# Kernel tuning notes

Hardware: AMD Instinct MI355X
Metric: run time of the kernel (lower is better)

The kernel has to match this reference:

```python
import jax, jax.numpy as jnp
import numpy as np

EPS = 1e-5

def _inorm(t):
    # InstanceNorm2d, affine=False: normalize each (B,C) plane over H,W
    m = t.mean((2, 3), keepdims=True)
    v = t.var((2, 3), keepdims=True)
    return (t - m) * jax.lax.rsqrt(v + EPS)

def _conv(x, w, b):
    y = jax.lax.conv_general_dilated(x, w, (1, 1), 'SAME',
        dimension_numbers=('NCHW', 'OIHW', 'NCHW'))
    return y + b[None, :, None, None]

def _ss2d(xh, in_proj_w, conv_w, conv_b, x_proj_w, dt_w, dt_b, A_logs, Ds,
          out_norm_g, out_norm_b, out_proj_w):
    # xh: (B,H,W,C) -> (B,H,W,C). VMamba-style 4-direction selective scan.
    B, H, W, C = xh.shape
    Di = in_proj_w.shape[0] // 2
    n = A_logs.shape[-1]
    R = dt_w.shape[-1]
    L = H * W
    xz = xh @ in_proj_w.T                      # (B,H,W,2*Di)
    xin, z = xz[..., :Di], xz[..., Di:]
    xc = xin.transpose(0, 3, 1, 2)             # (B,Di,H,W)
    xc = jax.lax.conv_general_dilated(xc, conv_w, (1, 1), 'SAME',
        feature_group_count=Di, dimension_numbers=('NCHW', 'OIHW', 'NCHW'))
    xc = jax.nn.silu(xc + conv_b[None, :, None, None])
    x1 = xc.reshape(B, Di, L)                  # row-major scan
    x2 = xc.transpose(0, 1, 3, 2).reshape(B, Di, L)  # col-major scan
    xs = jnp.stack([x1, x2, x1[..., ::-1], x2[..., ::-1]], axis=1)  # (B,4,Di,L)
    x_dbl = jnp.einsum('bkdl,kcd->bkcl', xs, x_proj_w)
    dts = jnp.einsum('bkrl,kdr->bkdl', x_dbl[:, :, :R], dt_w)
    Bs, Cs = x_dbl[:, :, R:R + n], x_dbl[:, :, R + n:]
    delta = jax.nn.softplus(dts + dt_b[None, :, :, None])
    A = -jnp.exp(A_logs)                       # (4,Di,n)
    scan_in = (jnp.moveaxis(xs, -1, 0), jnp.moveaxis(delta, -1, 0),
               jnp.moveaxis(Bs, -1, 0), jnp.moveaxis(Cs, -1, 0))
    def step(h, inp):
        u, d, b, c = inp                       # u,d:(B,4,Di)  b,c:(B,4,n)
        h = jnp.exp(d[..., None] * A) * h + (d * u)[..., None] * b[:, :, None, :]
        return h, (h * c[:, :, None, :]).sum(-1)
    h0 = jnp.zeros((B, 4, Di, n), xh.dtype)
    _, ys = jax.lax.scan(step, h0, scan_in)    # ys: (L,B,4,Di)
    out_y = jnp.moveaxis(ys, 0, -1) + Ds[None, :, :, None] * xs  # (B,4,Di,L)
    def _wh(t):
        return t.reshape(B, Di, W, H).transpose(0, 1, 3, 2).reshape(B, Di, L)
    y = out_y[:, 0] + out_y[:, 2, :, ::-1] + _wh(out_y[:, 1]) + _wh(out_y[:, 3, :, ::-1])
    y = y.transpose(0, 2, 1).reshape(B, H, W, Di)
    mu = y.mean(-1, keepdims=True)
    v = y.var(-1, keepdims=True)
    y = (y - mu) * jax.lax.rsqrt(v + EPS) * out_norm_g + out_norm_b
    return (y * jax.nn.silu(z)) @ out_proj_w.T

def setup_inputs():
    key = jax.random.key(0)
    ks = jax.random.split(key, 16)
    B, C, H, W = 4, 96, 64, 64
    Di, n, R, K, SQ, CC = 192, 8, 6, 4, 16, 16
    f = jnp.float32
    nrm = lambda k, s: 0.02 * jax.random.normal(k, s, dtype=f)
    inp = {}
    inp['x'] = jax.random.normal(ks[0], (B, C, H, W), dtype=f)
    inp['dz'] = jax.random.uniform(ks[1], (B, 1, H, W), dtype=f)
    inp['in_proj_w'] = nrm(ks[2], (2 * Di, C))
    inp['conv_w'] = nrm(ks[3], (Di, 1, 3, 3))
    inp['conv_b'] = jnp.zeros((Di,), f)
    inp['x_proj_w'] = nrm(ks[4], (K, R + 2 * n, Di))
    inp['dt_w'] = nrm(ks[5], (K, Di, R))
    inp['dt_b'] = 0.01 * jnp.ones((K, Di), f)
    inp['A_logs'] = jnp.log(jnp.tile(jnp.arange(1, n + 1, dtype=f)[None, None, :], (K, Di, 1)))
    inp['Ds'] = jnp.ones((K, Di), f)
    inp['out_norm_g'] = jnp.ones((Di,), f)
    inp['out_norm_b'] = jnp.zeros((Di,), f)
    inp['out_proj_w'] = nrm(ks[6], (C, Di))
    inp['ln_g'] = jnp.ones((C,), f)
    inp['ln_b'] = jnp.zeros((C,), f)
    inp['skip_ss2d'] = jnp.ones((C,), f)
    inp['cca_w1'] = nrm(ks[7], (SQ, C))
    inp['cca_b1'] = jnp.zeros((SQ,), f)
    inp['cca_w2'] = nrm(ks[8], (C, SQ))
    inp['cca_b2'] = jnp.zeros((C,), f)
    inp['bnc_w1'] = nrm(ks[9], (CC, C, 1, 1))
    inp['bnc_b1'] = jnp.zeros((CC,), f)
    inp['bnc_w2'] = nrm(ks[10], (CC, CC, 3, 3))
    inp['bnc_b2'] = jnp.zeros((CC,), f)
    inp['bnc_w3'] = nrm(ks[11], (C, CC, 1, 1))
    inp['bnc_b3'] = jnp.zeros((C,), f)
    return inp

def reference(x, dz, in_proj_w, conv_w, conv_b, x_proj_w, dt_w, dt_b, A_logs, Ds,
              out_norm_g, out_norm_b, out_proj_w, ln_g, ln_b, skip_ss2d,
              cca_w1, cca_b1, cca_w2, cca_b2,
              bnc_w1, bnc_b1, bnc_w2, bnc_b2, bnc_w3, bnc_b3):
    SKIP_CCA, SKIP_BNC = 0.4, 1.0
    # 1) channel cross-attention block (dz-guided SE), residual w/ skip 0.4
    xn = _inorm(x)
    pooled = (xn * dz).sum((2, 3)) / (dz.sum((2, 3)) + 1e-6)  # (B,C)
    s = jax.nn.sigmoid(jax.nn.relu(pooled @ cca_w1.T + cca_b1) @ cca_w2.T + cca_b2)
    x = xn * s[:, :, None, None] + SKIP_CCA * x
    # 2) SS2D block in NHWC, residual w/ learned per-channel skip weight
    xh = x.transpose(0, 2, 3, 1)
    mu = xh.mean(-1, keepdims=True)
    v = xh.var(-1, keepdims=True)
    xln = (xh - mu) * jax.lax.rsqrt(v + EPS) * ln_g + ln_b
    y = _ss2d(xln, in_proj_w, conv_w, conv_b, x_proj_w, dt_w, dt_b, A_logs, Ds,
              out_norm_g, out_norm_b, out_proj_w)
    x = (y + skip_ss2d * xh).transpose(0, 3, 1, 2)
    # 3) bottleneck conv block, residual w/ skip 1.0
    xn = _inorm(x)
    h = jax.nn.relu(_conv(xn, bnc_w1, bnc_b1))
    h = jax.nn.relu(_conv(h, bnc_w2, bnc_b2))
    h = _conv(h, bnc_w3, bnc_b3)
    return h + SKIP_BNC * x
```

## Files before the change

kernel.cpp:

```cpp
#include <hip/hip_runtime.h>
#include <hip/hip_bf16.h>
#include <math.h>

constexpr int TOT_IN = 1685008;

constexpr size_t F_x    = 64;
constexpr size_t F_dz   = F_x + 1572864;
constexpr size_t F_ipw  = F_dz + 16384;
constexpr size_t F_convw= F_ipw + 36864;
constexpr size_t F_convb= F_convw + 1728;
constexpr size_t F_xpw  = F_convb + 192;
constexpr size_t F_dtw  = F_xpw + 16896;
constexpr size_t F_dtb  = F_dtw + 4608;
constexpr size_t F_alog = F_dtb + 768;
constexpr size_t F_Dsv  = F_alog + 6144;
constexpr size_t F_ong  = F_Dsv + 768;
constexpr size_t F_onb  = F_ong + 192;
constexpr size_t F_opw  = F_onb + 192;
constexpr size_t F_lng  = F_opw + 18432;
constexpr size_t F_lnb  = F_lng + 96;
constexpr size_t F_skip = F_lnb + 96;
constexpr size_t F_cw1  = F_skip + 96;
constexpr size_t F_cb1  = F_cw1 + 1536;
constexpr size_t F_cw2  = F_cb1 + 16;
constexpr size_t F_cb2  = F_cw2 + 1536;
constexpr size_t F_bw1  = F_cb2 + 96;
constexpr size_t F_bb1  = F_bw1 + 1536;
constexpr size_t F_bw2  = F_bb1 + 16;
constexpr size_t F_bb2  = F_bw2 + 2304;
constexpr size_t F_bw3  = F_bb2 + 16;
constexpr size_t F_bb3  = F_bw3 + 1536;
constexpr size_t F_stat = 1685504;
constexpr size_t F_mean1= F_stat;
constexpr size_t F_rstd1= F_stat + 384;
constexpr size_t F_wsum = F_stat + 768;
constexpr size_t F_sca  = F_stat + 1216;
constexpr size_t F_mean2= F_stat + 1664;
constexpr size_t F_rstd2= F_stat + 2048;
constexpr size_t F_xcca = 1689600;
constexpr size_t F_xln  = F_xcca + 1572864;
constexpr size_t F_xin  = F_xln  + 1572864;
constexpr size_t F_z    = F_xin  + 3145728;
constexpr size_t F_xct  = F_z    + 3145728;
constexpr size_t F_xdbl = F_xct  + 3145728;
constexpr size_t F_old1 = F_xdbl + 1572864;
constexpr size_t F_xccaT= F_old1 + 3145728;
constexpr size_t F_yc   = F_xccaT+ 1572864;
constexpr size_t F_tb   = F_yc   + 3145728;
constexpr size_t F_x2   = F_tb   + 3145728;
constexpr size_t F_h1   = F_x2   + 1572864;
constexpr size_t F_h2   = F_h1   + 262144;
constexpr size_t F_xpwt = F_h2   + 262144;
constexpr size_t F_ipwt = F_xpwt + 18432;
constexpr size_t F_opwt = F_ipwt + 36864;
constexpr size_t F_cwt  = F_opwt + 18432;
constexpr size_t F_hend = F_xin;
constexpr size_t F_apr  = F_tb;
constexpr size_t F_hcar = F_old1;

__constant__ int g_off[27] = {
  0,1572864,1589248,1626112,1627840,1628032,1644928,1649536,1650304,1656448,
  1657216,1657408,1657600,1676032,1676128,1676224,1676320,1677856,1677872,1679408,
  1679504,1681040,1681056,1683360,1683376,1684912,1685008};

struct Ptrs26 { const void* p[26]; };

static __device__ __forceinline__ float sigmoidf_(float x){ return 1.f/(1.f+__expf(-x)); }
static __device__ __forceinline__ float siluf_(float x){ return x*sigmoidf_(x); }
static __device__ __forceinline__ float softplusf_(float x){ return x>15.f ? x : log1pf(__expf(x)); }
static __device__ __forceinline__ int mapk_(int k,int l){
  switch(k){
    case 0: return l;
    case 1: return ((l&63)<<6)|(l>>6);
    case 2: return 4095-l;
    default:{ int l2=4095-l; return ((l2&63)<<6)|(l2>>6); }
  }
}

__global__ void k_convert(Ptrs26 ps, float* __restrict__ F){
  int bf = (((const unsigned int*)ps.p[9])[0] == 0x3F803F80u) ? 1 : 0;
  int stride = gridDim.x*blockDim.x;
  for (int idx = blockIdx.x*blockDim.x+threadIdx.x; idx < TOT_IN; idx += stride){
    int lo = 0, hi = 26;
    while (hi - lo > 1){ int mid = (lo+hi)>>1; if (idx >= g_off[mid]) lo = mid; else hi = mid; }
    int s = lo;
    int loc = idx - g_off[s];
    float v;
    if (bf) v = __bfloat162float(((const __hip_bfloat16*)ps.p[s])[loc]);
    else    v = ((const float*)ps.p[s])[loc];
    F[64 + idx] = v;
  }
}

__global__ void k_wtrans(float* __restrict__ F){
  int idx = blockIdx.x*256 + threadIdx.x;
  if (idx < 18432){
    int c = idx % 24; int d = (idx/24) % 192; int k = idx/(24*192);
    F[F_xpwt + idx] = (c < 22) ? F[F_xpw + (size_t)(k*22 + c)*192 + d] : 0.f;
  } else if (idx < 18432 + 36864){
    int i = idx - 18432;
    int j = i % 384, c = i / 384;
    F[F_ipwt + i] = F[F_ipw + (size_t)j*96 + c];
  } else if (idx < 18432 + 36864 + 18432){
    int i = idx - 18432 - 36864;
    int c = i % 96, d = i / 96;
    F[F_opwt + i] = F[F_opw + (size_t)c*192 + d];
  } else if (idx < 18432 + 36864 + 18432 + 1728){
    int i = idx - 18432 - 36864 - 18432;
    int d = i % 192, tap = i / 192;
    F[F_cwt + i] = F[F_convw + (size_t)d*9 + tap];
  }
}

__global__ void k_inorm1(float* __restrict__ F){
  int bc = blockIdx.x; int b = bc/96;
  const float* xp  = F + F_x  + (size_t)bc*4096;
  const float* dzp = F + F_dz + (size_t)b*4096;
  float s=0.f, s2=0.f, sw=0.f;
  for (int l=threadIdx.x; l<4096; l+=256){ float v=xp[l]; s+=v; s2+=v*v; sw+=v*dzp[l]; }
  for (int m=32;m;m>>=1){ s+=__shfl_xor(s,m); s2+=__shfl_xor(s2,m); sw+=__shfl_xor(sw,m); }
  __shared__ float red[12];
  int wid = threadIdx.x>>6;
  if ((threadIdx.x&63)==0){ red[wid]=s; red[4+wid]=s2; red[8+wid]=sw; }
  __syncthreads();
  if (threadIdx.x==0){
    s = red[0]+red[1]+red[2]+red[3];
    s2= red[4]+red[5]+red[6]+red[7];
    sw= red[8]+red[9]+red[10]+red[11];
    float mean = s*(1.f/4096.f);
    float var  = s2*(1.f/4096.f) - mean*mean;
    F[F_mean1+bc]=mean; F[F_rstd1+bc]=rsqrtf(var+1e-5f); F[F_wsum+bc]=sw;
  }
}

__global__ void k_cca(float* __restrict__ F){
  __shared__ float ps[96], hid[16], red[2];
  int b = blockIdx.x, t = threadIdx.x;
  const float* dzp = F + F_dz + (size_t)b*4096;
  float s=0.f;
  for (int l=t; l<4096; l+=128) s += dzp[l];
  for (int m=32;m;m>>=1) s += __shfl_xor(s,m);
  if ((t&63)==0) red[t>>6] = s;
  __syncthreads();
  float dzs = red[0]+red[1];
  if (t<96){
    int bc = b*96+t;
    ps[t] = F[F_rstd1+bc]*(F[F_wsum+bc]-F[F_mean1+bc]*dzs)/(dzs+1e-6f);
  }
  __syncthreads();
  if (t<16){
    float a = F[F_cb1+t];
    for (int c=0;c<96;c++) a += ps[c]*F[F_cw1+t*96+c];
    hid[t] = fmaxf(a,0.f);
  }
  __syncthreads();
  if (t<96){
    float a = F[F_cb2+t];
    for (int j=0;j<16;j++) a += hid[j]*F[F_cw2+t*16+j];
    F[F_sca+b*96+t] = sigmoidf_(a);
  }
}

__global__ __launch_bounds__(256) void k_ccat(float* __restrict__ F){
  __shared__ float T[96*33];
  int b = blockIdx.x >> 7; int l0 = (blockIdx.x & 127)*32;
  for (int i = threadIdx.x; i < 3072; i += 256){
    int l = i & 31, c = i >> 5;
    int bc = b*96 + c;
    float v = F[F_x + (size_t)bc*4096 + l0 + l];
    float xv = (v - F[F_mean1+bc])*F[F_rstd1+bc]*F[F_sca+bc] + 0.4f*v;
    F[F_xcca + (size_t)bc*4096 + l0 + l] = xv;
    T[c*33 + l] = xv;
  }
  __syncthreads();
  for (int i = threadIdx.x; i < 3072; i += 256){
    int c = i % 96, l = i / 96;
    F[F_xccaT + ((size_t)(b*4096 + l0 + l))*96 + c] = T[c*33 + l];
  }
}

__global__ __launch_bounds__(128) void k_gemm1(
    const float* __restrict__ xt, const float* __restrict__ lng,
    const float* __restrict__ lnb, const float* __restrict__ wt1,
    float* __restrict__ xin, float* __restrict__ z)
{
  int lb = blockIdx.x & 127; int jc = blockIdx.x >> 7;
  int t = lb*128 + threadIdx.x;
  const float4* rp = (const float4*)(xt + (size_t)t*96);
  float s=0.f, s2=0.f;
  for (int c4=0; c4<24; c4++){
    float4 v = rp[c4];
    s  += v.x+v.y+v.z+v.w;
    s2 += v.x*v.x+v.y*v.y+v.z*v.z+v.w*v.w;
  }
  float mean = s*(1.f/96.f);
  float rstd = rsqrtf(s2*(1.f/96.f) - mean*mean + 1e-5f);
  const float4* gp = (const float4*)lng;
  const float4* bp = (const float4*)lnb;
  const float* wbase = wt1 + jc*24;
  float acc[24];
  #pragma unroll
  for (int j=0;j<24;j++) acc[j]=0.f;
  for (int c4=0; c4<24; c4++){
    float4 av = rp[c4]; float4 g = gp[c4]; float4 bb = bp[c4];
    float tv[4];
    tv[0] = (av.x-mean)*rstd*g.x + bb.x;
    tv[1] = (av.y-mean)*rstd*g.y + bb.y;
    tv[2] = (av.z-mean)*rstd*g.z + bb.z;
    tv[3] = (av.w-mean)*rstd*g.w + bb.w;
    #pragma unroll
    for (int cc=0; cc<4; cc++){
      const float* wr = wbase + (size_t)(c4*4+cc)*384;
      #pragma unroll
      for (int j=0;j<24;j++) acc[j] += tv[cc] * wr[j];
    }
  }
  float* op = (jc < 8) ? (xin + (size_t)t*192 + jc*24)
                       : (z   + (size_t)t*192 + (jc-8)*24);
  float4* o4 = (float4*)op;
  #pragma unroll
  for (int q=0;q<6;q++) o4[q] = make_float4(acc[q*4],acc[q*4+1],acc[q*4+2],acc[q*4+3]);
}

__global__ void k_dwconv(const float* __restrict__ xin, const float* __restrict__ cwt,
                         const float* __restrict__ cb, float* __restrict__ xct){
  int idx = blockIdx.x*256 + threadIdx.x;
  if (idx >= 786432) return;
  int d4 = idx % 48; int bl = idx / 48; int l = bl & 4095; int b = bl >> 12;
  int h = l >> 6, w = l & 63;
  const float4* xp = (const float4*)(xin + (size_t)b*4096*192);
  const float4* wp = (const float4*)cwt;
  float4 bias = ((const float4*)cb)[d4];
  float ax=bias.x, ay=bias.y, az=bias.z, aw=bias.w;
  #pragma unroll
  for (int ky=0; ky<3; ky++){
    int hh = h + ky - 1; if ((unsigned)hh > 63u) continue;
    #pragma unroll
    for (int kx=0; kx<3; kx++){
      int ww = w + kx - 1; if ((unsigned)ww > 63u) continue;
      float4 xv = xp[(size_t)(hh*64+ww)*48 + d4];
      float4 wv = wp[(ky*3+kx)*48 + d4];
      ax += xv.x*wv.x; ay += xv.y*wv.y; az += xv.z*wv.z; aw += xv.w*wv.w;
    }
  }
  float4 o;
  o.x = ax*sigmoidf_(ax); o.y = ay*sigmoidf_(ay);
  o.z = az*sigmoidf_(az); o.w = aw*sigmoidf_(aw);
  ((float4*)xct)[idx] = o;
}

__global__ __launch_bounds__(256) void k_xdbl(
    const float* __restrict__ xct, const float* __restrict__ wt,
    float* __restrict__ xdbl)
{
  int lb = blockIdx.x & 15; int bk = blockIdx.x >> 4;
  int b = bk >> 2, k = bk & 3;
  int l = lb*256 + threadIdx.x;
  int sp = mapk_(k, l);
  const float4* rp = (const float4*)(xct + ((size_t)b*4096 + sp)*192);
  const float* wk = wt + (size_t)k*192*24;
  float acc[24];
  #pragma unroll
  for (int c=0;c<24;c++) acc[c]=0.f;
  #pragma unroll 2
  for (int d4=0; d4<48; d4++){
    float4 av = rp[d4];
    #pragma unroll
    for (int j=0;j<4;j++){
      float ad = (j==0)?av.x:(j==1)?av.y:(j==2)?av.z:av.w;
      const float* wd = wk + (d4*4+j)*24;
      #pragma unroll
      for (int c=0;c<22;c++) acc[c] += ad * wd[c];
    }
  }
  acc[22]=0.f; acc[23]=0.f;
  float4* op = (float4*)(xdbl + ((size_t)bk*4096 + l)*24);
  #pragma unroll
  for (int q=0;q<6;q++) op[q] = make_float4(acc[q*4],acc[q*4+1],acc[q*4+2],acc[q*4+3]);
}

__global__ __launch_bounds__(192) void k_scan1(
    const float* __restrict__ xdbl, const float* __restrict__ xct,
    const float* __restrict__ alogs, const float* __restrict__ dtws,
    const float* __restrict__ dtbs,
    float* __restrict__ hend, float* __restrict__ apr)
{
  int chunk = blockIdx.x & 127; int bk = blockIdx.x >> 7;
  int b = bk >> 2, k = bk & 3; int d = threadIdx.x;
  const float* alog = alogs + (size_t)(k*192+d)*8;
  float A_[8], hh[8], ap[8];
  #pragma unroll
  for (int i=0;i<8;i++){ A_[i] = -__expf(alog[i]); hh[i]=0.f; ap[i]=1.f; }
  bool structured = fabsf(A_[0] + 1.f) < 1e-4f;
  #pragma unroll
  for (int i=1;i<8;i++) structured = structured && (fabsf(A_[i] - (float)(i+1)*A_[0]) <= 1e-4f*fabsf(A_[i]));
  float dtw_[6];
  #pragma unroll
  for (int r=0;r<6;r++) dtw_[r] = dtws[(size_t)(k*192+d)*6 + r];
  float dtb_ = dtbs[k*192 + d];
  const float* xB = xdbl + ((size_t)bk*4096 + chunk*32)*24;
  const float* xc = xct + (size_t)b*4096*192 + d;
  if (structured){
    #pragma unroll 4
    for (int s=0;s<32;s++){
      const float* xl = xB + s*24;
      float dt = dtb_;
      #pragma unroll
      for (int r=0;r<6;r++) dt += xl[r]*dtw_[r];
      int sp = mapk_(k, chunk*32+s);
      float u = xc[(size_t)sp*192];
      float t = __expf(dt);
      float a1 = __builtin_amdgcn_rcpf(1.f + t);
      float delta = (dt > 15.f) ? dt : __logf(1.f + t);
      float du = delta*u;
      float a = a1;
      #pragma unroll
      for (int i=0;i<8;i++){
        hh[i] = a*hh[i] + du*xl[6+i];
        ap[i] *= a;
        a *= a1;
      }
    }
  } else {
    for (int s=0;s<32;s++){
      const float* xl = xB + s*24;
      float dt = dtb_;
      #pragma unroll
      for (int r=0;r<6;r++) dt += xl[r]*dtw_[r];
      int sp = mapk_(k, chunk*32+s);
      float u = xc[(size_t)sp*192];
      float delta = softplusf_(dt);
      float du = delta*u;
      #pragma unroll
      for (int i=0;i<8;i++){
        float a = __expf(delta*A_[i]);
        hh[i] = a*hh[i] + du*xl[6+i];
        ap[i] *= a;
      }
    }
  }
  size_t base = ((size_t)(bk<<7) + chunk)*1536 + d*8;
  #pragma unroll
  for (int i=0;i<8;i++){ hend[base+i]=hh[i]; apr[base+i]=ap[i]; }
}

__global__ void k_carry(const float* __restrict__ hend, const float* __restrict__ apr,
                        float* __restrict__ hcar){
  int t = blockIdx.x*256 + threadIdx.x;
  if (t >= 16*1536) return;
  int di8 = t % 1536; int bk = t / 1536;
  float carry = 0.f;
  for (int c=0;c<128;c++){
    size_t idx = ((size_t)(bk<<7) + c)*1536 + di8;
    hcar[idx] = carry;
    carry = apr[idx]*carry + hend[idx];
  }
}

__global__ __launch_bounds__(192) void k_scan2(
    const float* __restrict__ xdbl, const float* __restrict__ xct,
    const float* __restrict__ alogs, const float* __restrict__ dtws,
    const float* __restrict__ dtbs, const float* __restrict__ Dsv,
    const float* __restrict__ hcar, float* __restrict__ ycg)
{
  int chunk = blockIdx.x & 127; int bk = blockIdx.x >> 7;
  int b = bk >> 2, k = bk & 3; int d = threadIdx.x;
  const float* alog = alogs + (size_t)(k*192+d)*8;
  float A_[8], hh[8];
  size_t cb = ((size_t)(bk<<7) + chunk)*1536 + d*8;
  #pragma unroll
  for (int i=0;i<8;i++){ A_[i] = -__expf(alog[i]); hh[i] = hcar[cb+i]; }
  bool structured = fabsf(A_[0] + 1.f) < 1e-4f;
  #pragma unroll
  for (int i=1;i<8;i++) structured = structured && (fabsf(A_[i] - (float)(i+1)*A_[0]) <= 1e-4f*fabsf(A_[i]));
  float dtw_[6];
  #pragma unroll
  for (int r=0;r<6;r++) dtw_[r] = dtws[(size_t)(k*192+d)*6 + r];
  float dtb_ = dtbs[k*192 + d];
  float Dsc  = Dsv[k*192 + d];
  const float* xB = xdbl + ((size_t)bk*4096 + chunk*32)*24;
  const float* xc = xct + (size_t)b*4096*192 + d;
  float* yc = ycg + (size_t)b*4096*192 + d;
  if (structured){
    #pragma unroll 4
    for (int s=0;s<32;s++){
      const float* xl = xB + s*24;
      float dt = dtb_;
      #pragma unroll
      for (int r=0;r<6;r++) dt += xl[r]*dtw_[r];
      int sp = mapk_(k, chunk*32+s);
      float u = xc[(size_t)sp*192];
      float t = __expf(dt);
      float a1 = __builtin_amdgcn_rcpf(1.f + t);
      float delta = (dt > 15.f) ? dt : __logf(1.f + t);
      float du = delta*u;
      float a = a1, y = 0.f;
      #pragma unroll
      for (int i=0;i<8;i++){
        hh[i] = a*hh[i] + du*xl[6+i];
        y += hh[i]*xl[14+i];
        a *= a1;
      }
      atomicAdd(&yc[(size_t)sp*192], y + Dsc*u);
    }
  } else {
    for (int s=0;s<32;s++){
      const float* xl = xB + s*24;
      float dt = dtb_;
      #pragma unroll
      for (int r=0;r<6;r++) dt += xl[r]*dtw_[r];
      int sp = mapk_(k, chunk*32+s);
      float u = xc[(size_t)sp*192];
      float delta = softplusf_(dt);
      float du = delta*u;
      float y = 0.f;
      #pragma unroll
      for (int i=0;i<8;i++){
        float a = __expf(delta*A_[i]);
        hh[i] = a*hh[i] + du*xl[6+i];
        y += hh[i]*xl[14+i];
      }
      atomicAdd(&yc[(size_t)sp*192], y + Dsc*u);
    }
  }
}

__global__ void k_tnorm(float* __restrict__ F){
  int wid = threadIdx.x >> 6, lane = threadIdx.x & 63;
  int p = blockIdx.x*4 + wid;
  size_t base = (size_t)p*192;
  const float* yc = F + F_yc;
  float v[3]; float s=0.f, s2=0.f;
  #pragma unroll
  for (int j=0;j<3;j++){ v[j]=yc[base+j*64+lane]; s+=v[j]; s2+=v[j]*v[j]; }
  for (int m=32;m;m>>=1){ s+=__shfl_xor(s,m); s2+=__shfl_xor(s2,m); }
  float mean = s*(1.f/192.f);
  float rstd = rsqrtf(s2*(1.f/192.f) - mean*mean + 1e-5f);
  #pragma unroll
  for (int j=0;j<3;j++){
    int dd = j*64+lane;
    float zv = F[F_z + base + dd];
    float t = (v[j]-mean)*rstd*F[F_ong+dd] + F[F_onb+dd];
    F[F_tb + base + dd] = t * siluf_(zv);
  }
}

__global__ __launch_bounds__(128) void k_gemm2(
    const float* __restrict__ tb, const float* __restrict__ wt2,
    const float* __restrict__ skip, const float* __restrict__ xcca,
    float* __restrict__ x2)
{
  int lb = blockIdx.x & 127; int cbk = blockIdx.x >> 7;
  int t = lb*128 + threadIdx.x;
  int b = t >> 12, l = t & 4095;
  const float4* rp = (const float4*)(tb + (size_t)t*192);
  const float* wbase = wt2 + cbk*12;
  float acc[12];
  #pragma unroll
  for (int c=0;c<12;c++) acc[c]=0.f;
  #pragma unroll 2
  for (int d4=0; d4<48; d4++){
    float4 av = rp[d4];
    #pragma unroll
    for (int dd=0; dd<4; dd++){
      float ad = (dd==0)?av.x:(dd==1)?av.y:(dd==2)?av.z:av.w;
      const float* wr = wbase + (size_t)(d4*4+dd)*96;
      #pragma unroll
      for (int c=0;c<12;c++) acc[c] += ad * wr[c];
    }
  }
  #pragma unroll
  for (int c=0;c<12;c++){
    int cg = cbk*12 + c;
    size_t o = ((size_t)(b*96+cg))*4096 + l;
    x2[o] = acc[c] + skip[cg]*xcca[o];
  }
}

__global__ void k_inorm2(float* __restrict__ F){
  int bc = blockIdx.x;
  const float* xp = F + F_x2 + (size_t)bc*4096;
  float s=0.f, s2=0.f;
  for (int l=threadIdx.x; l<4096; l+=256){ float v=xp[l]; s+=v; s2+=v*v; }
  for (int m=32;m;m>>=1){ s+=__shfl_xor(s,m); s2+=__shfl_xor(s2,m); }
  __shared__ float red[8];
  int wid = threadIdx.x>>6;
  if ((threadIdx.x&63)==0){ red[wid]=s; red[4+wid]=s2; }
  __syncthreads();
  if (threadIdx.x==0){
    s = red[0]+red[1]+red[2]+red[3];
    s2= red[4]+red[5]+red[6]+red[7];
    float mean = s*(1.f/4096.f);
    float var  = s2*(1.f/4096.f) - mean*mean;
    F[F_mean2+bc]=mean; F[F_rstd2+bc]=rsqrtf(var+1e-5f);
  }
}

__global__ void k_bnc1(float* __restrict__ F){
  int idx = blockIdx.x*256 + threadIdx.x;
  if (idx >= 4*16*4096) return;
  int l = idx & 4095; int bj = idx >> 12; int j = bj % 16; int b = bj / 16;
  float acc = F[F_bb1 + j];
  const float* wp = F + F_bw1 + j*96;
  for (int c=0;c<96;c++){
    int bc = b*96+c;
    float xn = (F[F_x2 + (size_t)bc*4096 + l] - F[F_mean2+bc])*F[F_rstd2+bc];
    acc += xn*wp[c];
  }
  F[F_h1+idx] = fmaxf(acc, 0.f);
}

__global__ void k_bnc2(float* __restrict__ F){
  int idx = blockIdx.x*256 + threadIdx.x;
  if (idx >= 4*16*4096) return;
  int l = idx & 4095; int bj = idx >> 12; int j = bj % 16; int b = bj / 16;
  int h = l >> 6, w = l & 63;
  float acc = F[F_bb2 + j];
  const float* h1p = F + F_h1 + (size_t)b*16*4096;
  const float* wp  = F + F_bw2 + j*16*9;
  for (int jp=0; jp<16; jp++){
    #pragma unroll
    for (int ky=0; ky<3; ky++){
      int hh = h + ky - 1; if (hh < 0 || hh > 63) continue;
      #pragma unroll
      for (int kx=0; kx<3; kx++){
        int ww = w + kx - 1; if (ww < 0 || ww > 63) continue;
        acc += h1p[(size_t)jp*4096 + hh*64+ww] * wp[jp*9 + ky*3 + kx];
      }
    }
  }
  F[F_h2+idx] = fmaxf(acc, 0.f);
}

__global__ void k_bnc3(float* __restrict__ F, void* __restrict__ out, const unsigned int* __restrict__ ds){
  int idx = blockIdx.x*256 + threadIdx.x;
  if (idx >= 1572864) return;
  int l = idx & 4095; int bc = idx >> 12; int c = bc % 96; int b = bc / 96;
  float acc = F[F_bb3 + c];
  const float* h2p = F + F_h2 + (size_t)b*16*4096 + l;
  const float* wp  = F + F_bw3 + c*16;
  #pragma unroll
  for (int j=0;j<16;j++) acc += h2p[(size_t)j*4096]*wp[j];
  float res = acc + F[F_x2+idx];
  if (ds[0]==0x3F803F80u) ((__hip_bfloat16*)out)[idx] = __float2bfloat16(res);
  else                    ((float*)out)[idx] = res;
}

extern "C" void kernel_launch(void* const* d_in, const int* in_sizes, int n_in,
                              void* d_out, int out_size, void* d_ws, size_t ws_size,
                              hipStream_t stream) {
  (void)in_sizes; (void)n_in; (void)out_size; (void)ws_size;
  float* F = (float*)d_ws;

  Ptrs26 ps;
  for (int i=0;i<26;i++) ps.p[i] = d_in[i];

  k_convert<<<2048, 256, 0, stream>>>(ps, F);
  hipMemsetAsync((char*)d_ws + F_yc*sizeof(float), 0, 3145728*sizeof(float), stream);
  k_wtrans<<<296, 256, 0, stream>>>(F);

  k_inorm1<<<384, 256, 0, stream>>>(F);
  k_cca   <<<4,   128, 0, stream>>>(F);
  k_ccat  <<<512, 256, 0, stream>>>(F);
  k_gemm1 <<<2048,128, 0, stream>>>(F+F_xccaT, F+F_lng, F+F_lnb, F+F_ipwt, F+F_xin, F+F_z);
  k_dwconv<<<3072,256, 0, stream>>>(F+F_xin, F+F_cwt, F+F_convb, F+F_xct);
  k_xdbl  <<<256, 256, 0, stream>>>(F+F_xct, F+F_xpwt, F+F_xdbl);
  k_scan1 <<<2048,192, 0, stream>>>(F+F_xdbl, F+F_xct, F+F_alog, F+F_dtw, F+F_dtb,
                                    F+F_hend, F+F_apr);
  k_carry <<<96,  256, 0, stream>>>(F+F_hend, F+F_apr, F+F_hcar);
  k_scan2 <<<2048,192, 0, stream>>>(F+F_xdbl, F+F_xct, F+F_alog, F+F_dtw, F+F_dtb,
                                    F+F_Dsv, F+F_hcar, F+F_yc);
  k_tnorm <<<4096,256, 0, stream>>>(F);
  k_gemm2 <<<1024,128, 0, stream>>>(F+F_tb, F+F_opwt, F+F_skip, F+F_xcca, F+F_x2);
  k_inorm2<<<384, 256, 0, stream>>>(F);
  k_bnc1  <<<1024,256, 0, stream>>>(F);
  k_bnc2  <<<1024,256, 0, stream>>>(F);
  k_bnc3  <<<6144,256, 0, stream>>>(F, d_out, (const unsigned int*)d_in[9]);
}
```

Measured before the change: 385.3 us.

## Replace scan atomics with per-direction scan-order buffers summed in tnorm

Each direction of the selective scan now writes its output plainly, in scan order, into its own buffer instead of doing atomicAdd into a shared spatial buffer. The normalization kernel gathers the four directional contributions with the inverse index mappings and sums them. This removes the zero-fill memset and the atomic contention and scattered writes. The cost is extra workspace traffic, since tnorm reads four buffers instead of one. The hard-coded offsets reuse workspace regions (including xct, which tnorm then overwrites), so correctness depends on those regions being dead at that point.

```diff
diff --git a/kernel.cpp b/kernel.cpp
--- a/kernel.cpp
+++ b/kernel.cpp
@@ -58,6 +58,12 @@
 constexpr size_t F_apr  = F_tb;
 constexpr size_t F_hcar = F_old1;
 
+__constant__ int y4off[16] = {
+  3262464, 4048896, 4835328, 5621760, 6408192, 7194624,
+  18991104, 19777536,
+  20563968, 21350400, 22136832, 22923264,
+  23709696, 24496128, 25282560, 26068992};
+
 __constant__ int g_off[27] = {
   0,1572864,1589248,1626112,1627840,1628032,1644928,1649536,1650304,1656448,
   1657216,1657408,1657600,1676032,1676128,1676224,1676320,1677856,1677872,1679408,
@@ -361,7 +367,7 @@
     const float* __restrict__ xdbl, const float* __restrict__ xct,
     const float* __restrict__ alogs, const float* __restrict__ dtws,
     const float* __restrict__ dtbs, const float* __restrict__ Dsv,
-    const float* __restrict__ hcar, float* __restrict__ ycg)
+    const float* __restrict__ hcar, float* __restrict__ yout)
 {
   int chunk = blockIdx.x & 127; int bk = blockIdx.x >> 7;
   int b = bk >> 2, k = bk & 3; int d = threadIdx.x;
@@ -380,7 +386,7 @@
   float Dsc  = Dsv[k*192 + d];
   const float* xB = xdbl + ((size_t)bk*4096 + chunk*32)*24;
   const float* xc = xct + (size_t)b*4096*192 + d;
-  float* yc = ycg + (size_t)b*4096*192 + d;
+  float* yo = yout + (size_t)y4off[bk] + ((size_t)(chunk*32))*192 + d;
   if (structured){
     #pragma unroll 4
     for (int s=0;s<32;s++){
@@ -401,7 +407,7 @@
         y += hh[i]*xl[14+i];
         a *= a1;
       }
-      atomicAdd(&yc[(size_t)sp*192], y + Dsc*u);
+      yo[(size_t)s*192] = y + Dsc*u;
     }
   } else {
     for (int s=0;s<32;s++){
@@ -420,7 +426,7 @@
         hh[i] = a*hh[i] + du*xl[6+i];
         y += hh[i]*xl[14+i];
       }
-      atomicAdd(&yc[(size_t)sp*192], y + Dsc*u);
+      yo[(size_t)s*192] = y + Dsc*u;
     }
   }
 }
@@ -428,20 +434,29 @@
 __global__ void k_tnorm(float* __restrict__ F){
   int wid = threadIdx.x >> 6, lane = threadIdx.x & 63;
   int p = blockIdx.x*4 + wid;
-  size_t base = (size_t)p*192;
-  const float* yc = F + F_yc;
+  int b = p >> 12, sp = p & 4095;
+  int l1 = ((sp&63)<<6)|(sp>>6);
+  const float* y0 = F + (size_t)y4off[b*4+0] + (size_t)sp*192;
+  const float* y1 = F + (size_t)y4off[b*4+1] + (size_t)l1*192;
+  const float* y2 = F + (size_t)y4off[b*4+2] + (size_t)(4095-sp)*192;
+  const float* y3 = F + (size_t)y4off[b*4+3] + (size_t)(4095-l1)*192;
   float v[3]; float s=0.f, s2=0.f;
   #pragma unroll
-  for (int j=0;j<3;j++){ v[j]=yc[base+j*64+lane]; s+=v[j]; s2+=v[j]*v[j]; }
+  for (int j=0;j<3;j++){
+    int dd = j*64+lane;
+    v[j] = y0[dd] + y1[dd] + y2[dd] + y3[dd];
+    s += v[j]; s2 += v[j]*v[j];
+  }
   for (int m=32;m;m>>=1){ s+=__shfl_xor(s,m); s2+=__shfl_xor(s2,m); }
   float mean = s*(1.f/192.f);
   float rstd = rsqrtf(s2*(1.f/192.f) - mean*mean + 1e-5f);
+  size_t base = (size_t)p*192;
   #pragma unroll
   for (int j=0;j<3;j++){
     int dd = j*64+lane;
     float zv = F[F_z + base + dd];
     float t = (v[j]-mean)*rstd*F[F_ong+dd] + F[F_onb+dd];
-    F[F_tb + base + dd] = t * siluf_(zv);
+    F[F_xct + base + dd] = t * siluf_(zv);
   }
 }
 
@@ -556,7 +571,6 @@
   for (int i=0;i<26;i++) ps.p[i] = d_in[i];
 
   k_convert<<<2048, 256, 0, stream>>>(ps, F);
-  hipMemsetAsync((char*)d_ws + F_yc*sizeof(float), 0, 3145728*sizeof(float), stream);
   k_wtrans<<<296, 256, 0, stream>>>(F);
 
   k_inorm1<<<384, 256, 0, stream>>>(F);
@@ -569,9 +583,9 @@
                                     F+F_hend, F+F_apr);
   k_carry <<<96,  256, 0, stream>>>(F+F_hend, F+F_apr, F+F_hcar);
   k_scan2 <<<2048,192, 0, stream>>>(F+F_xdbl, F+F_xct, F+F_alog, F+F_dtw, F+F_dtb,
-                                    F+F_Dsv, F+F_hcar, F+F_yc);
+                                    F+F_Dsv, F+F_hcar, F);
   k_tnorm <<<4096,256, 0, stream>>>(F);
-  k_gemm2 <<<1024,128, 0, stream>>>(F+F_tb, F+F_opwt, F+F_skip, F+F_xcca, F+F_x2);
+  k_gemm2 <<<1024,128, 0, stream>>>(F+F_xct, F+F_opwt, F+F_skip, F+F_xcca, F+F_x2);
   k_inorm2<<<384, 256, 0, stream>>>(F);
   k_bnc1  <<<1024,256, 0, stream>>>(F);
   k_bnc2  <<<1024,256, 0, stream>>>(F);
```

New measurement: 379.4 us. Within noise of the previous version (-1.6%).
